# Optimization experiments

Measured on AMD Instinct MI355X. Metric: run time of the kernel, lower is better.

Reference implementation:

```python
import jax, jax.numpy as jnp
import numpy as np

D = 128           # embed_dim
NUM_LAYERS = 2
N_CLASSES = 4
OUT_CELL = 64
SPEAKERS = 2
INPUT_DIMS = [768, 74, 35]
B, T = 32, 60


def setup_inputs() -> dict:
    key = jax.random.key(0)
    ks = jax.random.split(key, 24)
    inp = {}
    inp['x0'] = jax.random.normal(ks[0], (B, T, INPUT_DIMS[0]), jnp.float32)
    inp['x1'] = jax.random.normal(ks[1], (B, T, INPUT_DIMS[1]), jnp.float32)
    inp['x2'] = jax.random.normal(ks[2], (B, T, INPUT_DIMS[2]), jnp.float32)
    inp['smask'] = jax.random.normal(ks[3], (B, T, SPEAKERS), jnp.float32)  # argmax -> speaker ids
    # modality projections
    for i, d in enumerate(INPUT_DIMS):
        inp[f'Wp{i}'] = jax.random.normal(ks[4 + i], (d, D), jnp.float32) / np.float32(np.sqrt(d))
        inp[f'bp{i}'] = jnp.zeros((D,), jnp.float32)
    # shared PositionEmbedding (ModuleList([m]*3) shares params)
    inp['freq_emb'] = jax.random.normal(ks[7], (SPEAKERS, D), jnp.float32) * 0.1
    inp['phase_emb'] = jax.random.normal(ks[8], (SPEAKERS, D), jnp.float32)
    # shared QRNNCell (ModuleList([cell]*num_layers) shares params)
    inp['U_x'] = jnp.linalg.qr(jax.random.normal(ks[9], (D, D), jnp.float32))[0]
    inp['U_h'] = jnp.linalg.qr(jax.random.normal(ks[10], (D, D), jnp.float32))[0]
    inp['Lambda'] = jnp.float32(0.5)
    # QMeasurement kernel (real/imag parts of D measurement vectors)
    inp['kernel_r'] = jnp.eye(D, dtype=jnp.float32) + 0.05 * jax.random.normal(ks[11], (D, D), jnp.float32)
    inp['kernel_i'] = 0.05 * jax.random.normal(ks[12], (D, D), jnp.float32)
    # SimpleNet fc_out
    inp['W1'] = jax.random.normal(ks[13], (D, OUT_CELL), jnp.float32) / np.float32(np.sqrt(D))
    inp['b1'] = jnp.zeros((OUT_CELL,), jnp.float32)
    inp['W2'] = jax.random.normal(ks[14], (OUT_CELL, N_CLASSES), jnp.float32) / np.float32(np.sqrt(OUT_CELL))
    inp['b2'] = jnp.zeros((N_CLASSES,), jnp.float32)
    return inp


def _qmn_forward(x0, x1, x2, smask, Wp0, bp0, Wp1, bp1, Wp2, bp2,
                 freq_emb, phase_emb, U_x, U_h, Lambda,
                 kernel_r, kernel_i, W1, b1, W2, b2):
    xs = [x0, x1, x2]
    Ws = [(Wp0, bp0), (Wp1, bp1), (Wp2, bp2)]
    reps = [jax.nn.relu(x @ W + b) for x, (W, b) in zip(xs, Ws)]           # [B,T,D] each
    # mixture weights: softmax over per-modality L2 norms
    norms = jnp.concatenate([jnp.linalg.norm(r, axis=-1, keepdims=True) for r in reps], axis=-1)
    weights = jax.nn.softmax(norms, axis=-1)                               # [B,T,M]
    # shared phase embedding: phase = t * freq[speaker] + phase[speaker]
    ids = jnp.argmax(smask, axis=-1)                                       # [B,T] int
    pos = jnp.arange(T, dtype=jnp.float32)[None, :, None]                  # [1,T,1]
    phase = pos * freq_emb[ids] + phase_emb[ids]                           # [B,T,D]
    cosp, sinp = jnp.cos(phase), jnp.sin(phase)
    # mixed density matrices rho = sum_m w_m |v_m><v_m|
    rho_r = jnp.zeros((B, T, D, D), jnp.float32)
    rho_i = jnp.zeros((B, T, D, D), jnp.float32)
    for m, r in enumerate(reps):
        a = r / jnp.maximum(jnp.linalg.norm(r, axis=-1, keepdims=True), 1e-12)
        pr = a * cosp                                                       # real amplitude
        pi = a * sinp                                                       # imag amplitude
        w = weights[..., m][..., None, None]
        rho_r = rho_r + w * (jnp.einsum('btm,btn->btmn', pr, pr) + jnp.einsum('btm,btn->btmn', pi, pi))
        rho_i = rho_i + w * (jnp.einsum('btm,btn->btmn', pi, pr) - jnp.einsum('btm,btn->btmn', pr, pi))
    # time-major for scan
    sr = jnp.transpose(rho_r, (1, 0, 2, 3))                                # [T,B,D,D]
    si = jnp.transpose(rho_i, (1, 0, 2, 3))

    def cell(h, x):
        hr, hi = h
        xr, xi = x
        Xr = jnp.einsum('mp,bpq,nq->bmn', U_x, xr, U_x)
        Xi = jnp.einsum('mp,bpq,nq->bmn', U_x, xi, U_x)
        Hr = jnp.einsum('mp,bpq,nq->bmn', U_h, hr, U_h)
        Hi = jnp.einsum('mp,bpq,nq->bmn', U_h, hi, U_h)
        nr = Lambda * Hr + (1.0 - Lambda) * Xr
        ni = Lambda * Hi + (1.0 - Lambda) * Xi
        return (nr, ni), (nr, ni)

    h0 = (jnp.broadcast_to(jnp.eye(D, dtype=jnp.float32) / D, (B, D, D)),
          jnp.zeros((B, D, D), jnp.float32))
    for _ in range(NUM_LAYERS):  # same shared cell params each layer
        _, (sr, si) = jax.lax.scan(cell, h0, (sr, si))
    # QMeasurement: p_k = Re(v_k^dag rho v_k), unit-norm complex measurement vectors
    nrm = jnp.sqrt(jnp.sum(kernel_r**2 + kernel_i**2, axis=1, keepdims=True))
    vr = kernel_r / jnp.maximum(nrm, 1e-12)                                # [K,D], K=D
    vi = kernel_i / jnp.maximum(nrm, 1e-12)
    probs = (jnp.einsum('tbmn,km,kn->tbk', sr, vr, vr)
             + jnp.einsum('tbmn,km,kn->tbk', sr, vi, vi)
             - jnp.einsum('tbmn,km,kn->tbk', si, vr, vi)
             + jnp.einsum('tbmn,km,kn->tbk', si, vi, vr))                  # [T,B,D]
    # SimpleNet (dropout = identity at inference)
    hid = jax.nn.relu(probs @ W1 + b1)
    out = jnp.tanh(hid @ W2 + b2)                                          # [T,B,C]
    out = jnp.transpose(out, (1, 0, 2))                                    # [B,T,C]
    return jax.nn.log_softmax(out, axis=2)


def reference(x0, x1, x2, smask, Wp0, bp0, Wp1, bp1, Wp2, bp2,
              freq_emb, phase_emb, U_x, U_h, Lambda,
              kernel_r, kernel_i, W1, b1, W2, b2):
    return _qmn_forward(x0, x1, x2, smask, Wp0, bp0, Wp1, bp1, Wp2, bp2,
                        freq_emb, phase_emb, U_x, U_h, Lambda,
                        kernel_r, kernel_i, W1, b1, W2, b2)
```

## Files before the change

kernel.cpp:

```cpp
#include <hip/hip_runtime.h>


#define DB 32
#define DT 60
#define DD 128
#define BT (DB*DT)
#define SP 136

typedef unsigned short ushort_t;
typedef __attribute__((ext_vector_type(8))) __bf16 bf16x8;
typedef __attribute__((ext_vector_type(8))) unsigned short ushort8_t;
typedef __attribute__((ext_vector_type(4))) float  float4v;

__device__ __forceinline__ float bf2f(ushort_t u){
  union { unsigned int i; float f; } x; x.i = ((unsigned int)u) << 16; return x.f;
}
__device__ __forceinline__ ushort_t f2bf(float f){
  union { float f; unsigned int i; } x; x.f = f;
  unsigned int lsb = (x.i >> 16) & 1u;
  return (ushort_t)((x.i + 0x7FFFu + lsb) >> 16);
}
__device__ __forceinline__ unsigned int f2bfpk(float a, float b){
#if defined(__gfx950__) && __has_builtin(__builtin_amdgcn_cvt_pk_bf16_f32)
  auto v = __builtin_amdgcn_cvt_pk_bf16_f32(a, b);
  unsigned int r; __builtin_memcpy(&r, &v, 4); return r;
#else
  return (unsigned int)f2bf(a) | ((unsigned int)f2bf(b) << 16);
#endif
}
__device__ __forceinline__ void split2(float v, ushort_t& h, ushort_t& l){
  h = f2bf(v); l = f2bf(v - bf2f(h));
}

template<int RT, int CT, bool ALO, bool BLO>
__device__ __forceinline__ void gemm_t(const ushort_t* Ah, const ushort_t* Al,
                                       const ushort_t* Bh, const ushort_t* Bl,
                                       float4v* acc, int row0, int col0, int gma, int q)
{
  for (int ks = 0; ks < 4; ks++){
    int ko = ks*32 + q*8;
    bf16x8 aF[RT], aL[RT], bF[CT], bL[CT];
    #pragma unroll
    for (int R = 0; R < RT; R++){
      int row = row0 + 16*R + gma;
      aF[R] = *(const bf16x8*)&Ah[row*SP + ko];
      if (ALO) aL[R] = *(const bf16x8*)&Al[row*SP + ko];
    }
    #pragma unroll
    for (int C = 0; C < CT; C++){
      int row = col0 + 16*C + gma;
      bF[C] = *(const bf16x8*)&Bh[row*SP + ko];
      if (BLO) bL[C] = *(const bf16x8*)&Bl[row*SP + ko];
    }
    #pragma unroll
    for (int R = 0; R < RT; R++)
      #pragma unroll
      for (int C = 0; C < CT; C++){
        float4v c = acc[R*CT+C];
        c = __builtin_amdgcn_mfma_f32_16x16x32_bf16(aF[R], bF[C], c, 0, 0, 0);
        if (BLO) c = __builtin_amdgcn_mfma_f32_16x16x32_bf16(aF[R], bL[C], c, 0, 0, 0);
        if (ALO) c = __builtin_amdgcn_mfma_f32_16x16x32_bf16(aL[R], bF[C], c, 0, 0, 0);
        acc[R*CT+C] = c;
      }
  }
}

template<int RT, int CT>
__device__ __forceinline__ void emit_t(const float4v* acc, ushort_t* dst, int stride,
                                       int row0, int col0, int gma, int q){
  #pragma unroll
  for (int R = 0; R < RT; R++)
    #pragma unroll
    for (int C = 0; C < CT; C++){
      int c = col0 + 16*C + gma, r0 = row0 + 16*R + 4*q;
      uint2 o;
      o.x = f2bfpk(acc[R*CT+C][0], acc[R*CT+C][1]);
      o.y = f2bfpk(acc[R*CT+C][2], acc[R*CT+C][3]);
      *(uint2*)&dst[(size_t)c*stride + r0] = o;
    }
}
template<int RT, int CT>
__device__ __forceinline__ void emit_split_t(const float4v* acc, ushort_t* dh, ushort_t* dl, int stride,
                                             int row0, int col0, int gma, int q){
  #pragma unroll
  for (int R = 0; R < RT; R++)
    #pragma unroll
    for (int C = 0; C < CT; C++){
      int c = col0 + 16*C + gma, r0 = row0 + 16*R + 4*q;
      ushort4 hh, ll;
      split2(acc[R*CT+C][0], hh.x, ll.x); split2(acc[R*CT+C][1], hh.y, ll.y);
      split2(acc[R*CT+C][2], hh.z, ll.z); split2(acc[R*CT+C][3], hh.w, ll.w);
      *(ushort4*)&dh[(size_t)c*stride + r0] = hh;
      *(ushort4*)&dl[(size_t)c*stride + r0] = ll;
    }
}
template<int NT>
__device__ __forceinline__ void lds_load_mat(ushort_t* dst, const ushort_t* src, int tid){
  for (int i = tid*8; i < 16384; i += NT*8){
    int r = i >> 7, k = i & 127;
    *(ushort8_t*)&dst[r*SP + k] = *(const ushort8_t*)&src[i];
  }
}
template<int NT>
__device__ __forceinline__ void lds_load_rows16(ushort_t* dst, const ushort_t* src, int tid){
  for (int i = tid*8; i < 2048; i += NT*8){
    int r = i >> 7, k = i & 127;
    *(ushort8_t*)&dst[r*SP + k] = *(const ushort8_t*)&src[i];
  }
}
template<int NT>
__device__ __forceinline__ void lds_load_mat2(ushort_t* d0, const ushort_t* s0,
                                              ushort_t* d1, const ushort_t* s1, int tid){
  constexpr int CH = 16384/(NT*8);
  ushort8_t r0[CH], r1[CH];
  #pragma unroll
  for (int c = 0; c < CH; c++) r0[c] = *(const ushort8_t*)&s0[tid*8 + c*NT*8];
  #pragma unroll
  for (int c = 0; c < CH; c++) r1[c] = *(const ushort8_t*)&s1[tid*8 + c*NT*8];
  #pragma unroll
  for (int c = 0; c < CH; c++){
    int i = tid*8 + c*NT*8; int r = i >> 7, k = i & 127;
    *(ushort8_t*)&d0[r*SP + k] = r0[c];
  }
  #pragma unroll
  for (int c = 0; c < CH; c++){
    int i = tid*8 + c*NT*8; int r = i >> 7, k = i & 127;
    *(ushort8_t*)&d1[r*SP + k] = r1[c];
  }
}
template<int NT>
__device__ __forceinline__ void lds_store_mat(ushort_t* dst, const ushort_t* src, int tid){
  for (int i = tid*8; i < 16384; i += NT*8){
    int r = i >> 7, k = i & 127;
    *(ushort8_t*)&dst[i] = *(const ushort8_t*)&src[r*SP + k];
  }
}

__global__ void k_small(const float* Ux, const float* Uh, const float* kr, const float* ki,
                        ushort_t* UxTh, ushort_t* UxTl, float* Vr, float* Vi,
                        ushort_t* PpH, ushort_t* PpL, ushort_t* PTh, ushort_t* PTl){
  int blk = blockIdx.x, d = threadIdx.x;
  if (blk < 128){
    int i = blk;
    float v = Ux[i*DD + d];
    ushort_t h, l; split2(v, h, l);
    UxTh[d*DD + i] = h; UxTl[d*DD + i] = l;
  } else if (blk < 256){
    __shared__ float red[DD];
    int k = blk - 128;
    float r = kr[k*DD+d], im = ki[k*DD+d];
    red[d] = r*r + im*im;
    __syncthreads();
    for (int s = 64; s > 0; s >>= 1){ if (d < s) red[d] += red[d+s]; __syncthreads(); }
    float nrm = fmaxf(sqrtf(red[0]), 1e-12f);
    Vr[k*DD+d] = r/nrm; Vi[k*DD+d] = im/nrm;
  } else {
    int i = blk - 256;
    float v = Uh[i*DD + d];
    ushort_t h, l; split2(v, h, l);
    PpH[i*DD + d] = h;  PpL[i*DD + d] = l;
    PTh[d*DD + i] = h;  PTl[d*DD + i] = l;
  }
}

__global__ __launch_bounds__(256,2) void k_pow2v2(ushort_t* PpH, ushort_t* PpL,
                                                  ushort_t* PTh, ushort_t* PTl, int s){
  __shared__ ushort_t Ah[128*SP], Al[128*SP], Bh[16*SP], Bl[16*SP];
  int blk = blockIdx.x;
  int which = blk >> 3, sl = blk & 7;
  size_t src = (size_t)(s-1)*16384, dst = (size_t)s*16384;
  int tid = threadIdx.x;
  int w = tid >> 6, lane = tid & 63, gma = lane & 15, q = lane >> 4;
  int row0 = 32*w;
  int gcol0 = sl*16;
  const ushort_t *A_h, *A_l, *B_h, *B_l; ushort_t *D_h, *D_l;
  if (which == 0){ A_h = PTh+src; A_l = PTl+src; B_h = PpH+src; B_l = PpL+src;
                   D_h = PpH+dst; D_l = PpL+dst; }
  else           { A_h = PpH+src; A_l = PpL+src; B_h = PTh+src; B_l = PTl+src;
                   D_h = PTh+dst; D_l = PTl+dst; }
  lds_load_mat<256>(Ah, A_h, tid);
  lds_load_mat<256>(Al, A_l, tid);
  lds_load_rows16<256>(Bh, B_h + (size_t)gcol0*128, tid);
  lds_load_rows16<256>(Bl, B_l + (size_t)gcol0*128, tid);
  __syncthreads();
  float4v acc[2];
  acc[0] = (float4v){0.f,0.f,0.f,0.f};
  acc[1] = (float4v){0.f,0.f,0.f,0.f};
  gemm_t<2,1,true,true>(Ah, Al, Bh, Bl, acc, row0, 0, gma, q);
  emit_split_t<2,1>(acc, D_h, D_l, 128, row0, gcol0, gma, q);
}

__global__ __launch_bounds__(512,1) void k_gchain(const ushort_t* PpH, const ushort_t* PpL,
                                                  const ushort_t* PTh, const ushort_t* PTl,
                                                  ushort_t* GTh, ushort_t* GTl){
  __shared__ ushort_t Ah[128*SP], Al[128*SP], Bh[128*SP], Bl[128*SP];
  int t = blockIdx.x;
  int tid = threadIdx.x;
  int w = tid >> 6, lane = tid & 63, gma = lane & 15, q = lane >> 4;
  int row0 = 32*(w >> 1), col0 = 64*(w & 1);
  size_t gslot = (size_t)t * 16384;
  if (t == 0){
    for (int i = tid*4; i < 16384; i += 2048){
      int r = i >> 7, k = i & 127;
      ushort4 zz; zz.x = zz.y = zz.z = zz.w = 0;
      *(ushort4*)&GTl[gslot + i] = zz;
      ushort4 oh;
      oh.x = (r == (k+0)) ? (ushort_t)0x3F80 : (ushort_t)0;
      oh.y = (r == (k+1)) ? (ushort_t)0x3F80 : (ushort_t)0;
      oh.z = (r == (k+2)) ? (ushort_t)0x3F80 : (ushort_t)0;
      oh.w = (r == (k+3)) ? (ushort_t)0x3F80 : (ushort_t)0;
      *(ushort4*)&GTh[gslot + i] = oh;
    }
    return;
  }
  int b0 = __ffs(t) - 1;
  int rem = t & ~(1 << b0);
  if (rem == 0){
    size_t ps = (size_t)b0 * 16384;
    for (int i = tid*4; i < 16384; i += 2048){
      *(ushort4*)&GTh[gslot + i] = *(const ushort4*)&PTh[ps + i];
      *(ushort4*)&GTl[gslot + i] = *(const ushort4*)&PTl[ps + i];
    }
    return;
  }
  lds_load_mat<512>(Ah, PpH + (size_t)b0*16384, tid);
  lds_load_mat<512>(Al, PpL + (size_t)b0*16384, tid);
  while (rem){
    int k = __ffs(rem) - 1;
    rem &= ~(1 << k);
    lds_load_mat<512>(Bh, PTh + (size_t)k*16384, tid);
    lds_load_mat<512>(Bl, PTl + (size_t)k*16384, tid);
    __syncthreads();
    float4v acc[8];
    #pragma unroll
    for (int i = 0; i < 8; i++) acc[i] = (float4v){0.f,0.f,0.f,0.f};
    if (rem){
      gemm_t<2,4,true,true>(Bh, Bl, Ah, Al, acc, row0, col0, gma, q);
      __syncthreads();
      emit_split_t<2,4>(acc, Ah, Al, SP, row0, col0, gma, q);
      __syncthreads();
    } else {
      gemm_t<2,4,true,true>(Ah, Al, Bh, Bl, acc, row0, col0, gma, q);
      emit_split_t<2,4>(acc, GTh + gslot, GTl + gslot, 128, row0, col0, gma, q);
    }
  }
}

__global__ __launch_bounds__(256,1) void k_precompMW(const ushort_t* GTh, const ushort_t* GTl,
                                                     const ushort_t* UxTh, const ushort_t* UxTl,
                                                     const float* Vr, const float* Vi,
                                                     ushort_t* Mh, ushort_t* Wh){
  __shared__ ushort_t Bh[128*SP], Bl[128*SP], Ah[128*SP], Al[128*SP];
  int blk = blockIdx.x;
  int tid = threadIdx.x;
  int w = tid >> 6, lane = tid & 63, gma = lane & 15, q = lane >> 4;
  int row0 = 64*(w >> 1), col0 = 64*(w & 1);
  if (blk < 60){
    int t = blk;
    lds_load_mat<256>(Bh, GTh + (size_t)t*16384, tid);
    lds_load_mat<256>(Bl, GTl + (size_t)t*16384, tid);
    lds_load_mat<256>(Ah, UxTh, tid);
    lds_load_mat<256>(Al, UxTl, tid);
    __syncthreads();
    float4v acc[16];
    #pragma unroll
    for (int i = 0; i < 16; i++) acc[i] = (float4v){0.f,0.f,0.f,0.f};
    gemm_t<4,4,true,true>(Ah, Al, Bh, Bl, acc, row0, col0, gma, q);
    __syncthreads();
    emit_split_t<4,4>(acc, Ah, Al, SP, row0, col0, gma, q);
    __syncthreads();
    #pragma unroll
    for (int i = 0; i < 16; i++) acc[i] = (float4v){0.f,0.f,0.f,0.f};
    gemm_t<4,4,true,true>(Bh, Bl, Ah, Al, acc, row0, col0, gma, q);
    #pragma unroll
    for (int R = 0; R < 4; R++)
      #pragma unroll
      for (int C = 0; C < 4; C++){
        int c = col0 + 16*C + gma, r0 = row0 + 16*R + 4*q;
        uint2 o;
        o.x = f2bfpk(acc[R*4+C][0], acc[R*4+C][1]);
        o.y = f2bfpk(acc[R*4+C][2], acc[R*4+C][3]);
        *(uint2*)&Mh[(size_t)t*16384 + c*128 + r0] = o;
      }
  } else {
    int bx = blk - 60;
    int t = bx >> 1, which = bx & 1;
    lds_load_mat<256>(Ah, GTh + (size_t)t*16384, tid);
    lds_load_mat<256>(Al, GTl + (size_t)t*16384, tid);
    const float* V = which ? Vi : Vr;
    for (int i = tid; i < 16384; i += 256){
      int r = i >> 7, k = i & 127;
      ushort_t h, l; split2(V[i], h, l);
      Bh[r*SP + k] = h; Bl[r*SP + k] = l;
    }
    __syncthreads();
    float4v acc[16];
    #pragma unroll
    for (int i = 0; i < 16; i++) acc[i] = (float4v){0.f,0.f,0.f,0.f};
    gemm_t<4,4,true,true>(Ah, Al, Bh, Bl, acc, row0, col0, gma, q);
    #pragma unroll
    for (int R = 0; R < 4; R++)
      #pragma unroll
      for (int C = 0; C < 4; C++){
        int c = col0 + 16*C + gma, r0 = row0 + 16*R + 4*q;
        uint2 o;
        o.x = f2bfpk(acc[R*4+C][0], acc[R*4+C][1]);
        o.y = f2bfpk(acc[R*4+C][2], acc[R*4+C][3]);
        *(uint2*)&Wh[(size_t)bx*16384 + c*128 + r0] = o;
      }
  }
}

__global__ __launch_bounds__(128) void k_prep(
    const float* x0, const float* x1, const float* x2, const float* smask,
    const float* Wp0, const float* bp0, const float* Wp1, const float* bp1,
    const float* Wp2, const float* bp2, const float* freq, const float* phem,
    const float* Ux, float* Q, float* Wgt)
{
  __shared__ float xs[768+74+35];
  __shared__ float red[DD];
  __shared__ float nrm3[3];
  __shared__ float ps[6][DD];
  int bt = blockIdx.x; int t = bt % DT;
  int d = threadIdx.x;
  const float* r0 = x0 + (size_t)bt*768;
  for (int k = d; k < 768; k += DD) xs[k] = r0[k];
  const float* r1 = x1 + (size_t)bt*74;
  if (d < 74) xs[768+d] = r1[d];
  const float* r2 = x2 + (size_t)bt*35;
  if (d < 35) xs[768+74+d] = r2[d];
  __syncthreads();
  float rep[3];
  { float acc = bp0[d]; for (int k = 0; k < 768; k++) acc += xs[k]*Wp0[k*DD+d]; rep[0] = fmaxf(acc, 0.f); }
  { float acc = bp1[d]; for (int k = 0; k < 74; k++) acc += xs[768+k]*Wp1[k*DD+d]; rep[1] = fmaxf(acc, 0.f); }
  { float acc = bp2[d]; for (int k = 0; k < 35; k++) acc += xs[768+74+k]*Wp2[k*DD+d]; rep[2] = fmaxf(acc, 0.f); }
  for (int m = 0; m < 3; m++){
    red[d] = rep[m]*rep[m];
    __syncthreads();
    for (int s = 64; s > 0; s >>= 1){ if (d < s) red[d] += red[d+s]; __syncthreads(); }
    if (d == 0) nrm3[m] = sqrtf(red[0]);
    __syncthreads();
  }
  float n0 = nrm3[0], n1 = nrm3[1], n2 = nrm3[2];
  float mx = fmaxf(n0, fmaxf(n1, n2));
  float e0 = expf(n0-mx), e1 = expf(n1-mx), e2 = expf(n2-mx);
  float einv = 1.f/(e0+e1+e2);
  if (d < 3) Wgt[bt*3+d] = (d==0?e0:(d==1?e1:e2))*einv;
  float s0 = smask[bt*2], s1 = smask[bt*2+1];
  int id = (s1 > s0) ? 1 : 0;
  float ph = (float)t * freq[id*DD+d] + phem[id*DD+d];
  float cp = cosf(ph), sp = sinf(ph);
  for (int m = 0; m < 3; m++){
    float a = rep[m] / fmaxf(nrm3[m], 1e-12f);
    ps[m][d]   = a*cp;
    ps[3+m][d] = a*sp;
  }
  __syncthreads();
  float qv[6] = {0.f,0.f,0.f,0.f,0.f,0.f};
  const float* uxr = Ux + (size_t)d*DD;
  for (int p = 0; p < DD; p++){
    float u = uxr[p];
    #pragma unroll
    for (int j = 0; j < 6; j++) qv[j] += u * ps[j][p];
  }
  #pragma unroll
  for (int j = 0; j < 6; j++)
    Q[((size_t)(j*BT) + bt)*DD + d] = qv[j];
}

__global__ __launch_bounds__(512,1) void k_vtrans(const ushort_t* GTh, const float* Q, ushort_t* At){
  __shared__ ushort_t Ah[128*SP];
  __shared__ ushort_t Bs[192*SP];
  int t = blockIdx.x;
  int tid = threadIdx.x;
  int w = tid >> 6, lane = tid & 63, gma = lane & 15, q = lane >> 4;
  int row0 = (w & 3)*32, col0 = (w >> 2)*96;
  lds_load_mat<512>(Ah, GTh + (size_t)t*16384, tid);
  for (int i = tid*4; i < 192*128; i += 2048){
    int m = i >> 7, k = i & 127;
    int j = m >> 5, b = m & 31;
    const float* src = &Q[((size_t)(j*BT) + b*DT + t)*DD + k];
    uint2 o; o.x = f2bfpk(src[0], src[1]); o.y = f2bfpk(src[2], src[3]);
    *(uint2*)&Bs[m*SP + k] = o;
  }
  __syncthreads();
  float4v acc[12];
  #pragma unroll
  for (int i = 0; i < 12; i++) acc[i] = (float4v){0.f,0.f,0.f,0.f};
  gemm_t<2,6,false,false>(Ah, Ah, Bs, Bs, acc, row0, col0, gma, q);
  emit_t<2,6>(acc, At + (size_t)t*24576, 128, row0, col0, gma, q);
}

__global__ __launch_bounds__(256) void k_zbuild(ushort_t* S, const ushort_t* At,
                                                const float* Wgt, const float* lamp){
  __shared__ ushort_t As[6*DD];
  __shared__ float wl[3];
  int blk = blockIdx.x;
  int b = blk >> 4, slab = blk & 15;
  int tid = threadIdx.x;
  int r = slab*8 + (tid >> 5);
  int c0 = (tid & 31)*4;
  float lam = lamp[0];
  float z0=0.f, z1=0.f, z2=0.f, z3=0.f;
  size_t off = (size_t)slab*1024 + tid*4;
  for (int t = 0; t < DT; t++){
    __syncthreads();
    if (tid < 192){
      int i = tid*4;
      int jj = i >> 7, n = i & 127;
      *(ushort4*)&As[i] = *(const ushort4*)&At[(size_t)t*24576 + (jj*32 + b)*128 + n];
    }
    if (tid < 3) wl[tid] = Wgt[(b*DT + t)*3 + tid];
    __syncthreads();
    float ar[6];
    #pragma unroll
    for (int jj = 0; jj < 6; jj++) ar[jj] = bf2f(As[jj*128 + r]);
    float cb[6];
    cb[0] = wl[0]*(ar[0]+ar[3]); cb[1] = wl[1]*(ar[1]+ar[4]); cb[2] = wl[2]*(ar[2]+ar[5]);
    cb[3] = wl[0]*(ar[3]-ar[0]); cb[4] = wl[1]*(ar[4]-ar[1]); cb[5] = wl[2]*(ar[5]-ar[2]);
    float y0=0.f, y1=0.f, y2=0.f, y3=0.f;
    #pragma unroll
    for (int jj = 0; jj < 6; jj++){
      ushort4 a4 = *(const ushort4*)&As[jj*128 + c0];
      float w_ = cb[jj];
      y0 += w_*bf2f(a4.x); y1 += w_*bf2f(a4.y);
      y2 += w_*bf2f(a4.z); y3 += w_*bf2f(a4.w);
    }
    z0 = lam*z0 + y0; z1 = lam*z1 + y1;
    z2 = lam*z2 + y2; z3 = lam*z3 + y3;
    uint2 o; o.x = f2bfpk(z0, z1); o.y = f2bfpk(z2, z3);
    *(uint2*)&S[((size_t)(t*32 + b))*16384 + off] = o;
  }
}

__global__ __launch_bounds__(512,4) void k_conjmid(ushort_t* S, const ushort_t* Mh,
                                                   const float* lamp){
  __shared__ ushort_t Bh[128*SP], Zs[128*SP];
  int blk = blockIdx.x;
  int t = blk >> 5;
  size_t slot = (size_t)blk * 16384;
  int tid = threadIdx.x;
  int w = tid >> 6, lane = tid & 63, gma = lane & 15, q = lane >> 4;
  int row0 = 32*(w >> 1), col0 = 64*(w & 1);
  lds_load_mat2<512>(Zs, S + slot, Bh, Mh + (size_t)t*16384, tid);
  __syncthreads();
  float lam = lamp[0];
  float oml = 1.f - lam;
  float ct = powf(lam, (float)(t+1)) / 128.f;
  float4v acc[8];
  #pragma unroll
  for (int i = 0; i < 8; i++) acc[i] = (float4v){0.f,0.f,0.f,0.f};
  gemm_t<2,4,false,false>(Zs, Zs, Bh, Bh, acc, row0, col0, gma, q);
  __syncthreads();
  emit_t<2,4>(acc, Zs, SP, row0, col0, gma, q);
  __syncthreads();
  #pragma unroll
  for (int i = 0; i < 8; i++) acc[i] = (float4v){0.f,0.f,0.f,0.f};
  gemm_t<2,4,false,false>(Zs, Zs, Bh, Bh, acc, row0, col0, gma, q);
  __syncthreads();
  #pragma unroll
  for (int R = 0; R < 2; R++)
    #pragma unroll
    for (int C = 0; C < 4; C++){
      int c = col0 + 16*C + gma, r0 = row0 + 16*R + 4*q;
      float v0 = oml*acc[R*4+C][0] + ((c == r0+0) ? ct : 0.f);
      float v1 = oml*acc[R*4+C][1] + ((c == r0+1) ? ct : 0.f);
      float v2 = oml*acc[R*4+C][2] + ((c == r0+2) ? ct : 0.f);
      float v3 = oml*acc[R*4+C][3] + ((c == r0+3) ? ct : 0.f);
      uint2 o; o.x = f2bfpk(v0, v1); o.y = f2bfpk(v2, v3);
      *(uint2*)&Zs[(size_t)c*SP + r0] = o;
    }
  __syncthreads();
  lds_store_mat<512>(S + slot, Zs, tid);
}

__device__ __forceinline__ void prefix_phase(ushort8_t& buf, bool doload,
                                             const ushort_t* Snext, ushort_t* Scur,
                                             float* a, float lam){
  ushort8_t u = buf;
  if (doload) buf = *(const ushort8_t*)Snext;
  #pragma unroll
  for (int i = 0; i < 8; i++) a[i] = lam*a[i] + bf2f(u[i]);
  uint4 o;
  o.x = f2bfpk(a[0],a[1]); o.y = f2bfpk(a[2],a[3]);
  o.z = f2bfpk(a[4],a[5]); o.w = f2bfpk(a[6],a[7]);
  *(uint4*)Scur = o;
}
__global__ __launch_bounds__(128) void k_prefix(ushort_t* S, const float* lamp){
  int blk = blockIdx.x;
  int chain = blk >> 4, slab = blk & 15;
  int tid = threadIdx.x;
  size_t off = (size_t)slab*1024 + tid*8;
  float lam = lamp[0];
  float a[8];
  #pragma unroll
  for (int i = 0; i < 8; i++) a[i] = 0.f;
  size_t addr = (size_t)chain*16384 + off;
  const size_t step = (size_t)32*16384;
  ushort8_t b0 = *(const ushort8_t*)&S[addr];
  ushort8_t b1 = *(const ushort8_t*)&S[addr + step];
  ushort8_t b2 = *(const ushort8_t*)&S[addr + 2*step];
  ushort8_t b3 = *(const ushort8_t*)&S[addr + 3*step];
  for (int t = 0; t < DT; t += 4){
    prefix_phase(b0, t+4 < DT, &S[addr + 4*step], &S[addr], a, lam); addr += step;
    prefix_phase(b1, t+5 < DT, &S[addr + 4*step], &S[addr], a, lam); addr += step;
    prefix_phase(b2, t+6 < DT, &S[addr + 4*step], &S[addr], a, lam); addr += step;
    prefix_phase(b3, t+7 < DT, &S[addr + 4*step], &S[addr], a, lam); addr += step;
  }
}

__global__ __launch_bounds__(512,2) void k_meas(const ushort_t* S, const ushort_t* Wh,
                                                const float* lamp, float* Probs){
  __shared__ ushort_t Vs[128*SP], Cs[128*SP];
  __shared__ float Pd[64];
  int raw = blockIdx.x;
  int tb = (raw & 7) | ((raw >> 4) << 3);
  int h  = (raw >> 3) & 1;
  int t = tb >> 5;
  int tid = threadIdx.x;
  int w = tid >> 6, lane = tid & 63, gma = lane & 15, q = lane >> 4;
  int row0 = 16*(w >> 1);
  int col0 = 64*(w & 1);
  size_t slot = (size_t)tb * 16384;
  size_t wbase = (size_t)(t*2) * 16384;
  ushort8_t creg[4], vreg[4];
  #pragma unroll
  for (int c = 0; c < 4; c++)
    creg[c] = *(const ushort8_t*)&S[slot + tid*8 + c*4096];
  #pragma unroll
  for (int c = 0; c < 4; c++){
    int i = tid*8 + c*4096;
    int r = i >> 7, k = i & 127;
    size_t gsrc = wbase + ((r < 64) ? 0 : 16384) + (size_t)(64*h + (r & 63))*128 + k;
    vreg[c] = *(const ushort8_t*)&Wh[gsrc];
  }
  if (tid < 64) Pd[tid] = 0.f;
  #pragma unroll
  for (int c = 0; c < 4; c++){
    int i = tid*8 + c*4096;
    int r = i >> 7, k = i & 127;
    *(ushort8_t*)&Cs[r*SP + k] = creg[c];
  }
  #pragma unroll
  for (int c = 0; c < 4; c++){
    int i = tid*8 + c*4096;
    int r = i >> 7, k = i & 127;
    *(ushort8_t*)&Vs[r*SP + k] = vreg[c];
  }
  __syncthreads();
  float4v acc[8];
  #pragma unroll
  for (int i = 0; i < 8; i++) acc[i] = (float4v){0.f,0.f,0.f,0.f};
  #pragma unroll
  for (int ks = 0; ks < 4; ks++){
    int ko = ks*32 + q*8;
    bf16x8 aF0 = *(const bf16x8*)&Vs[(row0 + gma)*SP + ko];
    bf16x8 aF1 = *(const bf16x8*)&Vs[(row0 + 64 + gma)*SP + ko];
    bf16x8 bF[4];
    #pragma unroll
    for (int C = 0; C < 4; C++)
      bF[C] = *(const bf16x8*)&Cs[(col0 + 16*C + gma)*SP + ko];
    #pragma unroll
    for (int C = 0; C < 4; C++){
      acc[C]   = __builtin_amdgcn_mfma_f32_16x16x32_bf16(aF0, bF[C], acc[C],   0, 0, 0);
      acc[4+C] = __builtin_amdgcn_mfma_f32_16x16x32_bf16(aF1, bF[C], acc[4+C], 0, 0, 0);
    }
  }
  #pragma unroll
  for (int j = 0; j < 4; j++){
    int kr = row0 + 4*q + j;
    float s = 0.f;
    #pragma unroll
    for (int C = 0; C < 4; C++){
      int m = col0 + 16*C + gma;
      float w0 = bf2f(Vs[kr*SP + m]);
      float w1 = bf2f(Vs[(kr + 64)*SP + m]);
      s += acc[C][j]*(w0 + w1) + acc[4+C][j]*(w1 - w0);
    }
    #pragma unroll
    for (int off = 1; off < 16; off <<= 1)
      s += __shfl_xor(s, off, 64);
    if (gma == 0) atomicAdd(&Pd[kr], s);
  }
  __syncthreads();
  if (tid < 64){
    float lam = lamp[0];
    float ct = powf(lam, (float)(t+1)) / 128.f;
    Probs[(size_t)tb*DD + 64*h + tid] = (1.f - lam)*Pd[tid] + ct;
  }
}

__global__ __launch_bounds__(64) void k_head(const float* Probs, const float* W1, const float* b1,
                        const float* W2, const float* b2, float* out)
{
  __shared__ float ps[DD];
  __shared__ float hid[64];
  __shared__ float ov[4];
  int tb = blockIdx.x;
  int tid = threadIdx.x;
  ps[tid] = Probs[(size_t)tb*DD + tid];
  ps[tid+64] = Probs[(size_t)tb*DD + 64 + tid];
  __syncthreads();
  float acc = b1[tid];
  for (int dd = 0; dd < DD; dd++) acc += ps[dd]*W1[dd*64 + tid];
  hid[tid] = fmaxf(acc, 0.f);
  __syncthreads();
  if (tid < 4){
    float o = b2[tid];
    for (int j = 0; j < 64; j++) o += hid[j]*W2[j*4 + tid];
    ov[tid] = tanhf(o);
  }
  __syncthreads();
  if (tid == 0){
    float m = fmaxf(fmaxf(ov[0],ov[1]), fmaxf(ov[2],ov[3]));
    float lse = logf(expf(ov[0]-m)+expf(ov[1]-m)+expf(ov[2]-m)+expf(ov[3]-m));
    int t = tb >> 5, b = tb & 31;
    float* o = out + ((size_t)(b*DT + t))*4;
    o[0] = ov[0]-m-lse; o[1] = ov[1]-m-lse;
    o[2] = ov[2]-m-lse; o[3] = ov[3]-m-lse;
  }
}

extern "C" void kernel_launch(void* const* d_in, const int* in_sizes, int n_in,
                              void* d_out, int out_size, void* d_ws, size_t ws_size,
                              hipStream_t stream)
{
  const float* x0    = (const float*)d_in[0];
  const float* x1    = (const float*)d_in[1];
  const float* x2    = (const float*)d_in[2];
  const float* smask = (const float*)d_in[3];
  const float* Wp0   = (const float*)d_in[4];
  const float* bp0   = (const float*)d_in[5];
  const float* Wp1   = (const float*)d_in[6];
  const float* bp1   = (const float*)d_in[7];
  const float* Wp2   = (const float*)d_in[8];
  const float* bp2   = (const float*)d_in[9];
  const float* freq  = (const float*)d_in[10];
  const float* phem  = (const float*)d_in[11];
  const float* Ux    = (const float*)d_in[12];
  const float* Uh    = (const float*)d_in[13];
  const float* lamp  = (const float*)d_in[14];
  const float* kr    = (const float*)d_in[15];
  const float* ki    = (const float*)d_in[16];
  const float* W1    = (const float*)d_in[17];
  const float* b1    = (const float*)d_in[18];
  const float* W2    = (const float*)d_in[19];
  const float* b2    = (const float*)d_in[20];

  char* ws = (char*)d_ws;
  auto alignup = [](size_t x){ return (x + 255) & ~(size_t)255; };
  size_t off = 0;
  ushort_t* S   = (ushort_t*)(ws + off); off = alignup(off + (size_t)1920*16384*sizeof(ushort_t));
  float* Qbuf   = (float*)(ws + off);    off = alignup(off + (size_t)6*BT*DD*sizeof(float));
  float* Wgt    = (float*)(ws + off);    off = alignup(off + (size_t)BT*3*sizeof(float));
  float* Vr     = (float*)(ws + off);    off = alignup(off + (size_t)DD*DD*sizeof(float));
  float* Vi     = (float*)(ws + off);    off = alignup(off + (size_t)DD*DD*sizeof(float));
  ushort_t* UxTh = (ushort_t*)(ws + off); off = alignup(off + (size_t)DD*DD*sizeof(ushort_t));
  ushort_t* UxTl = (ushort_t*)(ws + off); off = alignup(off + (size_t)DD*DD*sizeof(ushort_t));
  float* Probs  = (float*)(ws + off);    off = alignup(off + (size_t)BT*DD*sizeof(float));
  ushort_t* PpH = (ushort_t*)(ws + off); off = alignup(off + (size_t)6*16384*sizeof(ushort_t));
  ushort_t* PpL = (ushort_t*)(ws + off); off = alignup(off + (size_t)6*16384*sizeof(ushort_t));
  ushort_t* PTh = (ushort_t*)(ws + off); off = alignup(off + (size_t)6*16384*sizeof(ushort_t));
  ushort_t* PTl = (ushort_t*)(ws + off); off = alignup(off + (size_t)6*16384*sizeof(ushort_t));
  ushort_t* Mh  = (ushort_t*)(ws + off); off = alignup(off + (size_t)60*16384*sizeof(ushort_t));
  ushort_t* Wmh = (ushort_t*)(ws + off); off = alignup(off + (size_t)120*16384*sizeof(ushort_t));
  ushort_t* GTh = (ushort_t*)(ws + off); off = alignup(off + (size_t)60*16384*sizeof(ushort_t));
  ushort_t* GTl = (ushort_t*)(ws + off); off = alignup(off + (size_t)60*16384*sizeof(ushort_t));
  ushort_t* At  = (ushort_t*)(ws + off); off = alignup(off + (size_t)60*24576*sizeof(ushort_t));
  (void)ws_size; (void)in_sizes; (void)n_in; (void)out_size;

  k_small<<<384, 128, 0, stream>>>(Ux, Uh, kr, ki, UxTh, UxTl, Vr, Vi, PpH, PpL, PTh, PTl);
  k_prep<<<BT, 128, 0, stream>>>(x0, x1, x2, smask, Wp0, bp0, Wp1, bp1, Wp2, bp2, freq, phem, Ux, Qbuf, Wgt);
  for (int s = 1; s <= 5; s++)
    k_pow2v2<<<16, 256, 0, stream>>>(PpH, PpL, PTh, PTl, s);
  k_gchain<<<60, 512, 0, stream>>>(PpH, PpL, PTh, PTl, GTh, GTl);
  k_precompMW<<<180, 256, 0, stream>>>(GTh, GTl, UxTh, UxTl, Vr, Vi, Mh, Wmh);
  k_vtrans<<<60, 512, 0, stream>>>(GTh, Qbuf, At);
  k_zbuild<<<512, 256, 0, stream>>>(S, At, Wgt, lamp);
  k_conjmid<<<1920, 512, 0, stream>>>(S, Mh, lamp);
  k_prefix<<<512, 128, 0, stream>>>(S, lamp);
  k_meas<<<3840, 512, 0, stream>>>(S, Wmh, lamp, Probs);
  k_head<<<BT, 64, 0, stream>>>(Probs, W1, b1, W2, b2, (float*)d_out);
}
```

Baseline: 351.9 us.

## Replace scalar prep kernel with split-bf16 MFMA projection and Ux GEMMs

The old per-row scalar kernel did the three modality projections and the Ux multiply with FP32 loops. It is now split into k_proj, which runs the projections as split-bf16 (hi/lo) MFMA GEMMs over 128-row tiles, k_mix, which computes norms, softmax weights and the phase modulation, and k_qtrans, which applies Ux by MFMA and emits bf16 Q directly. k_vtrans then loads bf16 Q with vector loads instead of converting from fp32. The change adds three launches and extra intermediate buffers, and the split-bf16 arithmetic may change numerics slightly.

```diff
diff --git a/kernel.cpp b/kernel.cpp
--- a/kernel.cpp
+++ b/kernel.cpp
@@ -137,8 +137,12 @@
 }
 
 __global__ void k_small(const float* Ux, const float* Uh, const float* kr, const float* ki,
-                        ushort_t* UxTh, ushort_t* UxTl, float* Vr, float* Vi,
-                        ushort_t* PpH, ushort_t* PpL, ushort_t* PTh, ushort_t* PTl){
+                        const float* Wp0, const float* Wp1, const float* Wp2,
+                        ushort_t* UxTh, ushort_t* UxTl, ushort_t* UxH, ushort_t* UxL,
+                        float* Vr, float* Vi,
+                        ushort_t* PpH, ushort_t* PpL, ushort_t* PTh, ushort_t* PTl,
+                        ushort_t* WT0h, ushort_t* WT0l, ushort_t* WT1h, ushort_t* WT1l,
+                        ushort_t* WT2h, ushort_t* WT2l){
   int blk = blockIdx.x, d = threadIdx.x;
   if (blk < 128){
     int i = blk;
@@ -154,13 +158,158 @@
     for (int s = 64; s > 0; s >>= 1){ if (d < s) red[d] += red[d+s]; __syncthreads(); }
     float nrm = fmaxf(sqrtf(red[0]), 1e-12f);
     Vr[k*DD+d] = r/nrm; Vi[k*DD+d] = im/nrm;
-  } else {
+  } else if (blk < 384){
     int i = blk - 256;
     float v = Uh[i*DD + d];
     ushort_t h, l; split2(v, h, l);
     PpH[i*DD + d] = h;  PpL[i*DD + d] = l;
     PTh[d*DD + i] = h;  PTl[d*DD + i] = l;
-  }
+  } else {
+    int dd2 = blk - 384;
+    ushort_t h, l;
+    for (int k = d; k < 768; k += 128){
+      split2(Wp0[(size_t)k*DD + dd2], h, l);
+      WT0h[(size_t)dd2*768 + k] = h; WT0l[(size_t)dd2*768 + k] = l;
+    }
+    { float v = (d < 74) ? Wp1[(size_t)d*DD + dd2] : 0.f;
+      split2(v, h, l); WT1h[dd2*128 + d] = h; WT1l[dd2*128 + d] = l; }
+    { float v = (d < 35) ? Wp2[(size_t)d*DD + dd2] : 0.f;
+      split2(v, h, l); WT2h[dd2*128 + d] = h; WT2l[dd2*128 + d] = l; }
+    { split2(Ux[(size_t)dd2*DD + d], h, l);
+      UxH[dd2*DD + d] = h; UxL[dd2*DD + d] = l; }
+  }
+}
+
+__global__ __launch_bounds__(512,1) void k_proj(
+    const float* x0, const float* x1, const float* x2,
+    const ushort_t* WT0h, const ushort_t* WT0l,
+    const ushort_t* WT1h, const ushort_t* WT1l,
+    const ushort_t* WT2h, const ushort_t* WT2l,
+    const float* bp0, const float* bp1, const float* bp2,
+    float* Reps)
+{
+  __shared__ ushort_t Ah[128*SP], Al[128*SP], Bh[128*SP], Bl[128*SP];
+  int blk = blockIdx.x;
+  int tile = blk / 3, m = blk % 3;
+  int bt0 = tile*128;
+  int tid = threadIdx.x;
+  int w = tid >> 6, lane = tid & 63, gma = lane & 15, q = lane >> 4;
+  int row0 = 32*(w >> 1), col0 = 64*(w & 1);
+  const float* xsrc = (m==0)? x0 : (m==1)? x1 : x2;
+  const ushort_t* Wh_ = (m==0)? WT0h : (m==1)? WT1h : WT2h;
+  const ushort_t* Wl_ = (m==0)? WT0l : (m==1)? WT1l : WT2l;
+  const float* bp = (m==0)? bp0 : (m==1)? bp1 : bp2;
+  int KW = (m==0)? 768 : (m==1)? 74 : 35;
+  int nch = (m==0)? 6 : 1;
+  int KWpad = (m==0)? 768 : 128;
+  float4v acc[8];
+  #pragma unroll
+  for (int i = 0; i < 8; i++) acc[i] = (float4v){0.f,0.f,0.f,0.f};
+  for (int ch = 0; ch < nch; ch++){
+    if (ch) __syncthreads();
+    for (int i = tid*8; i < 16384; i += 4096){
+      int r = i >> 7, k = i & 127;
+      *(ushort8_t*)&Ah[r*SP + k] = *(const ushort8_t*)&Wh_[(size_t)r*KWpad + ch*128 + k];
+      *(ushort8_t*)&Al[r*SP + k] = *(const ushort8_t*)&Wl_[(size_t)r*KWpad + ch*128 + k];
+    }
+    if (m == 0){
+      for (int i = tid*4; i < 16384; i += 2048){
+        int r = i >> 7, k = i & 127;
+        float4 v = *(const float4*)&xsrc[(size_t)(bt0 + r)*768 + ch*128 + k];
+        ushort4 hh, ll;
+        split2(v.x, hh.x, ll.x); split2(v.y, hh.y, ll.y);
+        split2(v.z, hh.z, ll.z); split2(v.w, hh.w, ll.w);
+        *(ushort4*)&Bh[r*SP + k] = hh;
+        *(ushort4*)&Bl[r*SP + k] = ll;
+      }
+    } else {
+      for (int i = tid; i < 16384; i += 512){
+        int r = i >> 7, k = i & 127;
+        float v = (k < KW) ? xsrc[(size_t)(bt0 + r)*KW + k] : 0.f;
+        ushort_t h, l; split2(v, h, l);
+        Bh[r*SP + k] = h; Bl[r*SP + k] = l;
+      }
+    }
+    __syncthreads();
+    gemm_t<2,4,true,true>(Ah, Al, Bh, Bl, acc, row0, col0, gma, q);
+  }
+  #pragma unroll
+  for (int R = 0; R < 2; R++){
+    int r0 = row0 + 16*R + 4*q;
+    float4 bv = *(const float4*)&bp[r0];
+    #pragma unroll
+    for (int C = 0; C < 4; C++){
+      int c = col0 + 16*C + gma;
+      float4v a = acc[R*4+C];
+      float4 o;
+      o.x = fmaxf(a[0]+bv.x, 0.f); o.y = fmaxf(a[1]+bv.y, 0.f);
+      o.z = fmaxf(a[2]+bv.z, 0.f); o.w = fmaxf(a[3]+bv.w, 0.f);
+      *(float4*)&Reps[(size_t)(bt0 + c)*384 + m*128 + r0] = o;
+    }
+  }
+}
+
+__global__ __launch_bounds__(128) void k_mix(const float* Reps, const float* smask,
+    const float* freq, const float* phem, ushort_t* PsH, ushort_t* PsL, float* Wgt)
+{
+  __shared__ float part[2][3];
+  int bt = blockIdx.x; int t = bt % DT;
+  int d = threadIdx.x;
+  float r0v = Reps[(size_t)bt*384 + d];
+  float r1v = Reps[(size_t)bt*384 + 128 + d];
+  float r2v = Reps[(size_t)bt*384 + 256 + d];
+  float s0 = r0v*r0v, s1 = r1v*r1v, s2 = r2v*r2v;
+  #pragma unroll
+  for (int off = 1; off < 64; off <<= 1){
+    s0 += __shfl_xor(s0, off, 64);
+    s1 += __shfl_xor(s1, off, 64);
+    s2 += __shfl_xor(s2, off, 64);
+  }
+  int wv = d >> 6;
+  if ((d & 63) == 0){ part[wv][0] = s0; part[wv][1] = s1; part[wv][2] = s2; }
+  __syncthreads();
+  float n0 = sqrtf(part[0][0] + part[1][0]);
+  float n1 = sqrtf(part[0][1] + part[1][1]);
+  float n2 = sqrtf(part[0][2] + part[1][2]);
+  float mx = fmaxf(n0, fmaxf(n1, n2));
+  float e0 = expf(n0-mx), e1 = expf(n1-mx), e2 = expf(n2-mx);
+  float einv = 1.f/(e0+e1+e2);
+  if (d < 3) Wgt[bt*3+d] = (d==0?e0:(d==1?e1:e2))*einv;
+  float sm0 = smask[bt*2], sm1 = smask[bt*2+1];
+  int id = (sm1 > sm0) ? 1 : 0;
+  float ph = (float)t * freq[id*DD+d] + phem[id*DD+d];
+  float cp = cosf(ph), sp = sinf(ph);
+  float a0 = r0v / fmaxf(n0, 1e-12f);
+  float a1 = r1v / fmaxf(n1, 1e-12f);
+  float a2 = r2v / fmaxf(n2, 1e-12f);
+  ushort_t h, l;
+  split2(a0*cp, h, l); PsH[((size_t)0*BT + bt)*DD + d] = h; PsL[((size_t)0*BT + bt)*DD + d] = l;
+  split2(a1*cp, h, l); PsH[((size_t)1*BT + bt)*DD + d] = h; PsL[((size_t)1*BT + bt)*DD + d] = l;
+  split2(a2*cp, h, l); PsH[((size_t)2*BT + bt)*DD + d] = h; PsL[((size_t)2*BT + bt)*DD + d] = l;
+  split2(a0*sp, h, l); PsH[((size_t)3*BT + bt)*DD + d] = h; PsL[((size_t)3*BT + bt)*DD + d] = l;
+  split2(a1*sp, h, l); PsH[((size_t)4*BT + bt)*DD + d] = h; PsL[((size_t)4*BT + bt)*DD + d] = l;
+  split2(a2*sp, h, l); PsH[((size_t)5*BT + bt)*DD + d] = h; PsL[((size_t)5*BT + bt)*DD + d] = l;
+}
+
+__global__ __launch_bounds__(512,1) void k_qtrans(const ushort_t* UxH, const ushort_t* UxL,
+                                                  const ushort_t* PsH, const ushort_t* PsL,
+                                                  ushort_t* Qb){
+  __shared__ ushort_t Ah[128*SP], Al[128*SP], Bh[128*SP], Bl[128*SP];
+  int blk = blockIdx.x;
+  int tid = threadIdx.x;
+  int w = tid >> 6, lane = tid & 63, gma = lane & 15, q = lane >> 4;
+  int row0 = 32*(w >> 1), col0 = 64*(w & 1);
+  size_t rbase = (size_t)blk*128*128;
+  lds_load_mat<512>(Ah, UxH, tid);
+  lds_load_mat<512>(Al, UxL, tid);
+  lds_load_mat<512>(Bh, PsH + rbase, tid);
+  lds_load_mat<512>(Bl, PsL + rbase, tid);
+  __syncthreads();
+  float4v acc[8];
+  #pragma unroll
+  for (int i = 0; i < 8; i++) acc[i] = (float4v){0.f,0.f,0.f,0.f};
+  gemm_t<2,4,true,true>(Ah, Al, Bh, Bl, acc, row0, col0, gma, q);
+  emit_t<2,4>(acc, Qb + rbase, 128, row0, col0, gma, q);
 }
 
 __global__ __launch_bounds__(256,2) void k_pow2v2(ushort_t* PpH, ushort_t* PpL,
@@ -311,64 +460,7 @@
   }
 }
 
-__global__ __launch_bounds__(128) void k_prep(
-    const float* x0, const float* x1, const float* x2, const float* smask,
-    const float* Wp0, const float* bp0, const float* Wp1, const float* bp1,
-    const float* Wp2, const float* bp2, const float* freq, const float* phem,
-    const float* Ux, float* Q, float* Wgt)
-{
-  __shared__ float xs[768+74+35];
-  __shared__ float red[DD];
-  __shared__ float nrm3[3];
-  __shared__ float ps[6][DD];
-  int bt = blockIdx.x; int t = bt % DT;
-  int d = threadIdx.x;
-  const float* r0 = x0 + (size_t)bt*768;
-  for (int k = d; k < 768; k += DD) xs[k] = r0[k];
-  const float* r1 = x1 + (size_t)bt*74;
-  if (d < 74) xs[768+d] = r1[d];
-  const float* r2 = x2 + (size_t)bt*35;
-  if (d < 35) xs[768+74+d] = r2[d];
-  __syncthreads();
-  float rep[3];
-  { float acc = bp0[d]; for (int k = 0; k < 768; k++) acc += xs[k]*Wp0[k*DD+d]; rep[0] = fmaxf(acc, 0.f); }
-  { float acc = bp1[d]; for (int k = 0; k < 74; k++) acc += xs[768+k]*Wp1[k*DD+d]; rep[1] = fmaxf(acc, 0.f); }
-  { float acc = bp2[d]; for (int k = 0; k < 35; k++) acc += xs[768+74+k]*Wp2[k*DD+d]; rep[2] = fmaxf(acc, 0.f); }
-  for (int m = 0; m < 3; m++){
-    red[d] = rep[m]*rep[m];
-    __syncthreads();
-    for (int s = 64; s > 0; s >>= 1){ if (d < s) red[d] += red[d+s]; __syncthreads(); }
-    if (d == 0) nrm3[m] = sqrtf(red[0]);
-    __syncthreads();
-  }
-  float n0 = nrm3[0], n1 = nrm3[1], n2 = nrm3[2];
-  float mx = fmaxf(n0, fmaxf(n1, n2));
-  float e0 = expf(n0-mx), e1 = expf(n1-mx), e2 = expf(n2-mx);
-  float einv = 1.f/(e0+e1+e2);
-  if (d < 3) Wgt[bt*3+d] = (d==0?e0:(d==1?e1:e2))*einv;
-  float s0 = smask[bt*2], s1 = smask[bt*2+1];
-  int id = (s1 > s0) ? 1 : 0;
-  float ph = (float)t * freq[id*DD+d] + phem[id*DD+d];
-  float cp = cosf(ph), sp = sinf(ph);
-  for (int m = 0; m < 3; m++){
-    float a = rep[m] / fmaxf(nrm3[m], 1e-12f);
-    ps[m][d]   = a*cp;
-    ps[3+m][d] = a*sp;
-  }
-  __syncthreads();
-  float qv[6] = {0.f,0.f,0.f,0.f,0.f,0.f};
-  const float* uxr = Ux + (size_t)d*DD;
-  for (int p = 0; p < DD; p++){
-    float u = uxr[p];
-    #pragma unroll
-    for (int j = 0; j < 6; j++) qv[j] += u * ps[j][p];
-  }
-  #pragma unroll
-  for (int j = 0; j < 6; j++)
-    Q[((size_t)(j*BT) + bt)*DD + d] = qv[j];
-}
-
-__global__ __launch_bounds__(512,1) void k_vtrans(const ushort_t* GTh, const float* Q, ushort_t* At){
+__global__ __launch_bounds__(512,1) void k_vtrans(const ushort_t* GTh, const ushort_t* Qb, ushort_t* At){
   __shared__ ushort_t Ah[128*SP];
   __shared__ ushort_t Bs[192*SP];
   int t = blockIdx.x;
@@ -376,12 +468,11 @@
   int w = tid >> 6, lane = tid & 63, gma = lane & 15, q = lane >> 4;
   int row0 = (w & 3)*32, col0 = (w >> 2)*96;
   lds_load_mat<512>(Ah, GTh + (size_t)t*16384, tid);
-  for (int i = tid*4; i < 192*128; i += 2048){
+  for (int i = tid*8; i < 192*128; i += 4096){
     int m = i >> 7, k = i & 127;
     int j = m >> 5, b = m & 31;
-    const float* src = &Q[((size_t)(j*BT) + b*DT + t)*DD + k];
-    uint2 o; o.x = f2bfpk(src[0], src[1]); o.y = f2bfpk(src[2], src[3]);
-    *(uint2*)&Bs[m*SP + k] = o;
+    *(ushort8_t*)&Bs[m*SP + k] =
+      *(const ushort8_t*)&Qb[((size_t)(j*BT) + b*DT + t)*DD + k];
   }
   __syncthreads();
   float4v acc[12];
@@ -651,12 +742,17 @@
   auto alignup = [](size_t x){ return (x + 255) & ~(size_t)255; };
   size_t off = 0;
   ushort_t* S   = (ushort_t*)(ws + off); off = alignup(off + (size_t)1920*16384*sizeof(ushort_t));
-  float* Qbuf   = (float*)(ws + off);    off = alignup(off + (size_t)6*BT*DD*sizeof(float));
+  ushort_t* Qb  = (ushort_t*)(ws + off); off = alignup(off + (size_t)6*BT*DD*sizeof(ushort_t));
+  float* Reps   = (float*)(ws + off);    off = alignup(off + (size_t)BT*384*sizeof(float));
+  ushort_t* PsH = (ushort_t*)(ws + off); off = alignup(off + (size_t)6*BT*DD*sizeof(ushort_t));
+  ushort_t* PsL = (ushort_t*)(ws + off); off = alignup(off + (size_t)6*BT*DD*sizeof(ushort_t));
   float* Wgt    = (float*)(ws + off);    off = alignup(off + (size_t)BT*3*sizeof(float));
   float* Vr     = (float*)(ws + off);    off = alignup(off + (size_t)DD*DD*sizeof(float));
   float* Vi     = (float*)(ws + off);    off = alignup(off + (size_t)DD*DD*sizeof(float));
   ushort_t* UxTh = (ushort_t*)(ws + off); off = alignup(off + (size_t)DD*DD*sizeof(ushort_t));
   ushort_t* UxTl = (ushort_t*)(ws + off); off = alignup(off + (size_t)DD*DD*sizeof(ushort_t));
+  ushort_t* UxH = (ushort_t*)(ws + off); off = alignup(off + (size_t)DD*DD*sizeof(ushort_t));
+  ushort_t* UxL = (ushort_t*)(ws + off); off = alignup(off + (size_t)DD*DD*sizeof(ushort_t));
   float* Probs  = (float*)(ws + off);    off = alignup(off + (size_t)BT*DD*sizeof(float));
   ushort_t* PpH = (ushort_t*)(ws + off); off = alignup(off + (size_t)6*16384*sizeof(ushort_t));
   ushort_t* PpL = (ushort_t*)(ws + off); off = alignup(off + (size_t)6*16384*sizeof(ushort_t));
@@ -667,15 +763,27 @@
   ushort_t* GTh = (ushort_t*)(ws + off); off = alignup(off + (size_t)60*16384*sizeof(ushort_t));
   ushort_t* GTl = (ushort_t*)(ws + off); off = alignup(off + (size_t)60*16384*sizeof(ushort_t));
   ushort_t* At  = (ushort_t*)(ws + off); off = alignup(off + (size_t)60*24576*sizeof(ushort_t));
+  ushort_t* WT0h = (ushort_t*)(ws + off); off = alignup(off + (size_t)128*768*sizeof(ushort_t));
+  ushort_t* WT0l = (ushort_t*)(ws + off); off = alignup(off + (size_t)128*768*sizeof(ushort_t));
+  ushort_t* WT1h = (ushort_t*)(ws + off); off = alignup(off + (size_t)128*128*sizeof(ushort_t));
+  ushort_t* WT1l = (ushort_t*)(ws + off); off = alignup(off + (size_t)128*128*sizeof(ushort_t));
+  ushort_t* WT2h = (ushort_t*)(ws + off); off = alignup(off + (size_t)128*128*sizeof(ushort_t));
+  ushort_t* WT2l = (ushort_t*)(ws + off); off = alignup(off + (size_t)128*128*sizeof(ushort_t));
   (void)ws_size; (void)in_sizes; (void)n_in; (void)out_size;
 
-  k_small<<<384, 128, 0, stream>>>(Ux, Uh, kr, ki, UxTh, UxTl, Vr, Vi, PpH, PpL, PTh, PTl);
-  k_prep<<<BT, 128, 0, stream>>>(x0, x1, x2, smask, Wp0, bp0, Wp1, bp1, Wp2, bp2, freq, phem, Ux, Qbuf, Wgt);
+  k_small<<<512, 128, 0, stream>>>(Ux, Uh, kr, ki, Wp0, Wp1, Wp2,
+                                   UxTh, UxTl, UxH, UxL, Vr, Vi,
+                                   PpH, PpL, PTh, PTl,
+                                   WT0h, WT0l, WT1h, WT1l, WT2h, WT2l);
+  k_proj<<<45, 512, 0, stream>>>(x0, x1, x2, WT0h, WT0l, WT1h, WT1l, WT2h, WT2l,
+                                 bp0, bp1, bp2, Reps);
+  k_mix<<<BT, 128, 0, stream>>>(Reps, smask, freq, phem, PsH, PsL, Wgt);
+  k_qtrans<<<90, 512, 0, stream>>>(UxH, UxL, PsH, PsL, Qb);
   for (int s = 1; s <= 5; s++)
     k_pow2v2<<<16, 256, 0, stream>>>(PpH, PpL, PTh, PTl, s);
   k_gchain<<<60, 512, 0, stream>>>(PpH, PpL, PTh, PTl, GTh, GTl);
   k_precompMW<<<180, 256, 0, stream>>>(GTh, GTl, UxTh, UxTl, Vr, Vi, Mh, Wmh);
-  k_vtrans<<<60, 512, 0, stream>>>(GTh, Qbuf, At);
+  k_vtrans<<<60, 512, 0, stream>>>(GTh, Qb, At);
   k_zbuild<<<512, 256, 0, stream>>>(S, At, Wgt, lamp);
   k_conjmid<<<1920, 512, 0, stream>>>(S, Mh, lamp);
   k_prefix<<<512, 128, 0, stream>>>(S, lamp);
```

New measurement: 361.2 us. 1.03x slower.
